# Kernel tuning notes

Measured on AMD Instinct MI355X. Metric: run time of the kernel, lower is better.

The kernel has to match this reference:

```python
import jax, jax.numpy as jnp
import numpy as np

DIM = 256
HEADS = 8
H = 32
W = 32
N = H * W  # must equal 4*DIM for the BatchNorm1d(dim*4) over the token dim to be valid
TAU = 2.0
V_TH = 1.0


def _rope_rotations():
    # RoPE buffer: shape (H, W, DIM//2) angles; k_max = DIM // (2*2)
    k_max = DIM // 4
    theta = 1.0 / (10000.0 ** (jnp.arange(k_max, dtype=jnp.float32) / k_max))
    hg, wg = jnp.meshgrid(jnp.arange(H, dtype=jnp.float32), jnp.arange(W, dtype=jnp.float32), indexing='ij')
    angles = jnp.concatenate([hg[..., None] * theta, wg[..., None] * theta], axis=-1)  # (H,W,DIM//2)
    return jnp.cos(angles), jnp.sin(angles)


def _apply_rope(x, cos, sin):
    # x: (b,H,W,DIM); complex rotation on consecutive (re,im) pairs
    x2 = x.reshape(*x.shape[:-1], -1, 2)
    re, im = x2[..., 0], x2[..., 1]
    out = jnp.stack([cos * re - sin * im, sin * re + cos * im], axis=-1)
    return out.reshape(x.shape)


def _lif(x):
    # MultiStepLIFNode(tau=2.0, detach_reset=True): time axis = axis 0 (here batch, as in source),
    # decay_input=True, v_reset=0 (hard reset), heaviside fwd + sigmoid(alpha=4) surrogate bwd.
    def step(v, xt):
        v = v + (xt - v) / TAU
        sg = jax.nn.sigmoid(4.0 * (v - V_TH))
        spike = jax.lax.stop_gradient((v >= V_TH).astype(x.dtype) - sg) + sg
        v = v * (1.0 - jax.lax.stop_gradient(spike))  # detach_reset hard reset to 0
        return v, spike
    _, s = jax.lax.scan(step, jnp.zeros_like(x[0]), x)
    return s


def setup_inputs() -> dict:
    key = jax.random.key(0)
    ks = jax.random.split(key, 4)
    x = jax.random.normal(ks[0], (8, N, DIM), dtype=jnp.float32)
    Wqk = jax.random.normal(ks[1], (DIM, 2 * DIM), dtype=jnp.float32) * 0.02
    bqk = jnp.zeros((2 * DIM,), dtype=jnp.float32)
    bn_gamma = jnp.ones((N,), dtype=jnp.float32)
    bn_beta = jnp.zeros((N,), dtype=jnp.float32)
    lepe_w = jax.random.normal(ks[2], (DIM, 1, 3, 3), dtype=jnp.float32) * 0.1
    lepe_b = jnp.zeros((DIM,), dtype=jnp.float32)
    return {"x": x, "Wqk": Wqk, "bqk": bqk, "bn_gamma": bn_gamma, "bn_beta": bn_beta,
            "lepe_w": lepe_w, "lepe_b": lepe_b}


def reference(x, Wqk, bqk, bn_gamma, bn_beta, lepe_w, lepe_b):
    b, n, c = x.shape
    hd = c // HEADS
    cos, sin = _rope_rotations()

    qk = x @ Wqk + bqk  # (b,n,2c)
    # Dropout is identity in eval. BatchNorm1d(4*dim) in eval mode: channels = token dim (n == 4*dim),
    # running_mean=0, running_var=1 -> pure affine per token index.
    qk = qk * bn_gamma[None, :, None] + bn_beta[None, :, None]
    qk = _lif(qk)
    q, k = qk[..., :c], qk[..., c:]  # reshape(b,n,2,c) split
    v = x
    q = jax.nn.elu(q) + 1.0
    k = jax.nn.elu(k) + 1.0

    q_rope = _apply_rope(q.reshape(b, H, W, c), cos, sin).reshape(b, n, HEADS, hd).transpose(0, 2, 1, 3)
    k_rope = _apply_rope(k.reshape(b, H, W, c), cos, sin).reshape(b, n, HEADS, hd).transpose(0, 2, 1, 3)
    qh = q.reshape(b, n, HEADS, hd).transpose(0, 2, 1, 3)  # (b,h,n,d)
    kh = k.reshape(b, n, HEADS, hd).transpose(0, 2, 1, 3)
    vh = v.reshape(b, n, HEADS, hd).transpose(0, 2, 1, 3)

    atten = jnp.einsum('bhnd,bhmd->bhnm', qh, kh)  # returned, not used for output
    kmean = kh.mean(axis=2, keepdims=True)  # (b,h,1,d)
    z = 1.0 / (jnp.einsum('bhnd,bhed->bhne', qh, kmean) + 1e-6)  # (b,h,n,1)
    kv = jnp.einsum('bhnd,bhne->bhde', k_rope, vh) / n  # (k^T n^-0.5) @ (v n^-0.5)
    out = jnp.einsum('bhnd,bhde->bhne', q_rope, kv) * z  # (b,h,n,d)
    out = out.transpose(0, 2, 1, 3).reshape(b, n, c)

    v_img = vh.transpose(0, 2, 1, 3).reshape(b, H, W, c).transpose(0, 3, 1, 2)  # (b,c,H,W)
    lepe = jax.lax.conv_general_dilated(v_img, lepe_w, (1, 1), 'SAME',
                                        feature_group_count=c,
                                        dimension_numbers=('NCHW', 'OIHW', 'NCHW'))
    lepe = lepe + lepe_b[None, :, None, None]
    out = out + lepe.transpose(0, 2, 3, 1).reshape(b, n, c)
    return (out, qh, kh, v_img, atten)
```

## Files before the change

kernel.cpp:

```cpp
#include <hip/hip_runtime.h>
#include <cstdint>
#include <cstddef>

#define OFF_OUT   0
#define OFF_QH    2097152
#define OFF_KH    4194304
#define OFF_VIMG  6291456
#define OFF_ATT   8388608

#define WS_MQ   0
#define WS_MK   65536
#define WS_TBL  131072
#define WS_KVP  393216
#define WS_KMP  655360

typedef float f32x4 __attribute__((ext_vector_type(4)));

__device__ __forceinline__ int wcol(int g) { return g * 8 + 4 * (g >> 2); }

__device__ __forceinline__ void gemm_lif_256(
    const float* __restrict__ x, const float* __restrict__ Wqk,
    const float* __restrict__ bqk, const float* __restrict__ gamma,
    const float* __restrict__ beta, unsigned* __restrict__ mq,
    unsigned* __restrict__ mk, float* pool,
    int blk_n, int blk_c, int t)
{
    const int ks = t >> 7, tl = t & 127;
    const int c_t = tl & 15, n_l = tl >> 4;
    const int n0 = blk_n * 8, c0 = blk_c * 128;
    float* wpool = pool + ks * 4480;
    float* xpool = pool + 8960 + ks * 2176;

    float acc[8][8];
    #pragma unroll
    for (int b = 0; b < 8; ++b)
        #pragma unroll
        for (int j = 0; j < 8; ++j) acc[b][j] = 0.f;

    const int um = tl >> 3, ukq = tl & 7;
    const float* gx0 = x + ((size_t)(um & 7) * 1024 + n0 + (um >> 3)) * 256
                         + ks * 128 + ukq * 4;
    const float* gw0 = Wqk + (size_t)(ks * 128 + (tl >> 5)) * 512 + c0 + (tl & 31) * 4;
    const int wg = (tl & 31) >> 1;
    float* lw_ = wpool + (tl >> 5) * 140 + wcol(wg) + (tl & 1) * 4;
    float* lx_ = xpool + (ukq * 4) * 68 + um;

    f32x4 px[4], pw[8];
    #pragma unroll
    for (int i = 0; i < 4; ++i) px[i] = *(const f32x4*)(gx0 + (size_t)(i * 2) * 256);
    #pragma unroll
    for (int i = 0; i < 8; ++i) pw[i] = *(const f32x4*)(gw0 + (size_t)(i * 4) * 512);

    for (int p = 0; p < 4; ++p) {
        #pragma unroll
        for (int i = 0; i < 4; ++i)
            #pragma unroll
            for (int j = 0; j < 4; ++j)
                lx_[j * 68 + i * 16] = px[i][j];
        #pragma unroll
        for (int i = 0; i < 8; ++i)
            *(f32x4*)(lw_ + i * 4 * 140) = pw[i];
        __syncthreads();
        if (p < 3) {
            int ko = (p + 1) * 32;
            #pragma unroll
            for (int i = 0; i < 4; ++i)
                px[i] = *(const f32x4*)(gx0 + (size_t)(i * 2) * 256 + ko);
            #pragma unroll
            for (int i = 0; i < 8; ++i)
                pw[i] = *(const f32x4*)(gw0 + (size_t)(ko + i * 4) * 512);
        }
        const int xc = n_l * 8;
        const int wc = wcol(c_t);
        #pragma unroll 8
        for (int kk = 0; kk < 32; ++kk) {
            f32x4 xa = *(const f32x4*)(xpool + kk * 68 + xc);
            f32x4 xb = *(const f32x4*)(xpool + kk * 68 + xc + 4);
            f32x4 wa = *(const f32x4*)(wpool + kk * 140 + wc);
            f32x4 wb = *(const f32x4*)(wpool + kk * 140 + wc + 4);
            #pragma unroll
            for (int b = 0; b < 4; ++b) {
                #pragma unroll
                for (int j = 0; j < 4; ++j) {
                    acc[b][j]         = fmaf(xa[b], wa[j], acc[b][j]);
                    acc[b][j + 4]     = fmaf(xa[b], wb[j], acc[b][j + 4]);
                    acc[b + 4][j]     = fmaf(xb[b], wa[j], acc[b + 4][j]);
                    acc[b + 4][j + 4] = fmaf(xb[b], wb[j], acc[b + 4][j + 4]);
                }
            }
        }
        __syncthreads();
    }

    float* comb = pool;
    if (ks == 1) {
        #pragma unroll
        for (int b = 0; b < 8; ++b)
            #pragma unroll
            for (int j = 0; j < 8; ++j)
                comb[(b * 8 + j) * 129 + tl] = acc[b][j];
    }
    __syncthreads();
    unsigned char* nib = (unsigned char*)(pool + 8960);
    if (ks == 0) {
        #pragma unroll
        for (int b = 0; b < 8; ++b)
            #pragma unroll
            for (int j = 0; j < 8; ++j)
                acc[b][j] += comb[(b * 8 + j) * 129 + tl];
        float g = gamma[n0 + n_l], be = beta[n0 + n_l];
        f32x4 bqa = *(const f32x4*)(bqk + c0 + c_t * 8);
        f32x4 bqb = *(const f32x4*)(bqk + c0 + c_t * 8 + 4);
        float v[8];
        #pragma unroll
        for (int j = 0; j < 8; ++j) v[j] = 0.f;
        #pragma unroll
        for (int b = 0; b < 8; ++b) {
            unsigned byte = 0;
            #pragma unroll
            for (int j = 0; j < 8; ++j) {
                float bqv = (j < 4) ? bqa[j] : bqb[j - 4];
                float a = (acc[b][j] + bqv) * g + be;
                v[j] = v[j] + (a - v[j]) * 0.5f;
                bool sp = (v[j] >= 1.f);
                v[j] = sp ? 0.f : v[j];
                byte |= (sp ? 1u : 0u) << j;
            }
            nib[n_l * 128 + c_t * 8 + b] = (unsigned char)byte;
        }
    }
    __syncthreads();
    {
        int b = t & 7, w = (t >> 3) & 3, nl = t >> 5;
        unsigned wd = 0;
        #pragma unroll
        for (int j = 0; j < 4; ++j)
            wd |= (unsigned)nib[nl * 128 + (w * 4 + j) * 8 + b] << (8 * j);
        unsigned h = (unsigned)((blk_c & 1) * 4 + w);
        unsigned* dst = (blk_c < 2) ? mq : mk;
        dst[b * 8192 + h * 1024 + n0 + nl] = wd;
    }
}

__global__ __launch_bounds__(256) void phaseA_kernel(
    const float* __restrict__ x, const float* __restrict__ Wqk,
    const float* __restrict__ bqk, const float* __restrict__ gamma,
    const float* __restrict__ beta, unsigned* __restrict__ mq,
    unsigned* __restrict__ mk, float* __restrict__ vimg,
    float* __restrict__ tbl)
{
    __shared__ float smem[13312];
    int t = threadIdx.x;
    int blk = blockIdx.x;
    if (blk < 256) {
        gemm_lif_256(x, Wqk, bqk, gamma, beta, mq, mk, smem,
                     blk >> 1, 2 + (blk & 1), t);
        return;
    }
    if (blk >= 2304) {
        int id = (blk - 2304) * 256 + t;
        int j = id & 127, n = id >> 7;
        int i = (j < 64) ? j : j - 64;
        float th = powf(10000.0f, -(float)i * (1.0f / 64.0f));
        float pos = (float)((j < 64) ? (n >> 5) : (n & 31));
        float ang = pos * th;
        tbl[n * 256 + j * 2]     = cosf(ang);
        tbl[n * 256 + j * 2 + 1] = sinf(ang);
        return;
    }
    float* s = smem;
    int tile = blk - 256;
    int b = tile >> 8, ti = tile & 255;
    int p0 = (ti >> 3) * 32, c0 = (ti & 7) * 32;
    int row = t >> 3, c4 = (t & 7) * 4;
    const float4 vl = *(const float4*)&x[(b * 1024 + p0 + row) * 256 + c0 + c4];
    s[row * 33 + c4 + 0] = vl.x; s[row * 33 + c4 + 1] = vl.y;
    s[row * 33 + c4 + 2] = vl.z; s[row * 33 + c4 + 3] = vl.w;
    __syncthreads();
    int cc = t >> 3, p4 = (t & 7) * 4;
    f32x4 o;
    o.x = s[(p4 + 0) * 33 + cc]; o.y = s[(p4 + 1) * 33 + cc];
    o.z = s[(p4 + 2) * 33 + cc]; o.w = s[(p4 + 3) * 33 + cc];
    *(f32x4*)&vimg[(b * 256 + c0 + cc) * 1024 + p0 + p4] = o;
}

__global__ __launch_bounds__(256) void phaseB_kernel(
    const float* __restrict__ x, const float* __restrict__ Wqk,
    const float* __restrict__ bqk, const float* __restrict__ gamma,
    const float* __restrict__ beta, unsigned* __restrict__ mq,
    unsigned* __restrict__ mk, const float* __restrict__ tbl,
    float* __restrict__ kvp, float* __restrict__ kmp)
{
    __shared__ float smem[13312];
    int t = threadIdx.x;
    int blk = blockIdx.x;
    if (blk < 256) {
        gemm_lif_256(x, Wqk, bqk, gamma, beta, mq, mk, smem,
                     blk >> 1, blk & 1, t);
        return;
    }
    int unit = blk - 256;
    int bh = unit >> 2, seg = unit & 3;
    int b = bh >> 3, h = bh & 7;
    int n0 = seg * 256;
    float* kr   = smem;
    float* vhs  = smem + 2304;
    float* part = smem + 4416;
    int d = t & 31, ch = t >> 5;
    int sc = 0;
    for (int i = 0; i < 32; ++i)
        sc += (mk[bh * 1024 + n0 + ch * 32 + i] >> d) & 1u;
    part[ch * 32 + d] = (float)sc;
    __syncthreads();
    if (t < 32) {
        float cs = 0.f;
        #pragma unroll
        for (int j = 0; j < 8; ++j) cs += part[j * 32 + t];
        kmp[bh * 128 + seg * 32 + t] = cs;
    }
    float a0 = 0, a1 = 0, a2 = 0, a3 = 0;
    int e = t & 31, db = (t >> 5) * 4;
    for (int c0 = n0; c0 < n0 + 256; c0 += 64) {
        __syncthreads();
        #pragma unroll
        for (int i = 0; i < 8; ++i) {
            int f = t + i * 256;
            int nn = f >> 5, dd = f & 31;
            int n = c0 + nn;
            unsigned w = mk[bh * 1024 + n];
            float kd = 1.0f + (float)((w >> dd) & 1u);
            float ko = 1.0f + (float)((w >> (dd ^ 1)) & 1u);
            const float* cp = tbl + n * 256 + h * 32 + (dd & ~1);
            float cc2 = cp[0], ss2 = cp[1];
            kr[nn * 36 + dd] = (dd & 1) ? (ss2 * ko + cc2 * kd) : (cc2 * kd - ss2 * ko);
            vhs[nn * 33 + dd] = x[(b * 1024 + n) * 256 + h * 32 + dd];
        }
        __syncthreads();
        #pragma unroll 8
        for (int nn = 0; nn < 64; ++nn) {
            float ve = vhs[nn * 33 + e];
            float4 kk = *(const float4*)&kr[nn * 36 + db];
            a0 = fmaf(kk.x, ve, a0); a1 = fmaf(kk.y, ve, a1);
            a2 = fmaf(kk.z, ve, a2); a3 = fmaf(kk.w, ve, a3);
        }
    }
    float* dst = kvp + bh * 4096 + seg * 1024;
    dst[(db + 0) * 32 + e] = a0;
    dst[(db + 1) * 32 + e] = a1;
    dst[(db + 2) * 32 + e] = a2;
    dst[(db + 3) * 32 + e] = a3;
}

__global__ __launch_bounds__(256) void phaseC_kernel(
    const unsigned* __restrict__ mq, const unsigned* __restrict__ mk,
    const float* __restrict__ x, const float* __restrict__ tbl,
    const float* __restrict__ kvp, const float* __restrict__ kmp,
    const float* __restrict__ lw, const float* __restrict__ lb,
    float* __restrict__ outbase)
{
    int t = threadIdx.x;
    if (blockIdx.x >= 512) {
        int blk = blockIdx.x - 512;
        int bh = blk >> 5;
        int tile = blk & 31;
        float* qh = outbase + OFF_QH;
        float* kh = outbase + OFF_KH;
        float* att = outbase + OFF_ATT;
        {
            int row = tile * 32 + (t >> 3);
            int d0 = (t & 7) * 4;
            unsigned wq = mq[bh * 1024 + row], wk = mk[bh * 1024 + row];
            f32x4 a, bb;
            a.x = 1.f + (float)((wq >> (d0 + 0)) & 1u);
            a.y = 1.f + (float)((wq >> (d0 + 1)) & 1u);
            a.z = 1.f + (float)((wq >> (d0 + 2)) & 1u);
            a.w = 1.f + (float)((wq >> (d0 + 3)) & 1u);
            bb.x = 1.f + (float)((wk >> (d0 + 0)) & 1u);
            bb.y = 1.f + (float)((wk >> (d0 + 1)) & 1u);
            bb.z = 1.f + (float)((wk >> (d0 + 2)) & 1u);
            bb.w = 1.f + (float)((wk >> (d0 + 3)) & 1u);
            *(f32x4*)&qh[((bh * 1024 + row) << 5) + d0] = a;
            *(f32x4*)&kh[((bh * 1024 + row) << 5) + d0] = bb;
        }
        uint4 mm = ((const uint4*)(mk + bh * 1024))[t];
        float4 rr;
        rr.x = (float)__popc(mm.x); rr.y = (float)__popc(mm.y);
        rr.z = (float)__popc(mm.z); rr.w = (float)__popc(mm.w);
        float* base = att + ((size_t)bh * 1024 + (size_t)tile * 32) * 1024;
        const unsigned* mqrow = mq + bh * 1024 + tile * 32;
        for (int row = 0; row < 32; ++row) {
            unsigned mqw = mqrow[row];
            float rq = 32.0f + (float)__popc(mqw);
            f32x4 o;
            o.x = rq + rr.x + (float)__popc(mqw & mm.x);
            o.y = rq + rr.y + (float)__popc(mqw & mm.y);
            o.z = rq + rr.z + (float)__popc(mqw & mm.z);
            o.w = rq + rr.w + (float)__popc(mqw & mm.w);
            ((f32x4*)(base + (size_t)row * 1024))[t] = o;
        }
        return;
    }
    int bi = blockIdx.x;
    int bh = bi >> 3, sub = bi & 7;
    int pseg = sub >> 1, half = sub & 1;
    int b = bh >> 3, h = bh & 7;
    bool hy = (h < 4);
    int e = t & 31, p_l = t >> 5;
    int p = pseg * 8 + p_l;
    int q0 = half * 16;
    float* out = outbase + OFF_OUT;

    __shared__ float kvs[32][32];
    __shared__ float kmf[32];
    __shared__ float zs[128];
    const float inv = 1.0f / 1024.0f;
    #pragma unroll
    for (int i = 0; i < 4; ++i) {
        int f = t + i * 256;
        const float* kp = kvp + bh * 4096 + f;
        kvs[f >> 5][f & 31] = (kp[0] + kp[1024] + kp[2048] + kp[3072]) * inv;
    }
    if (t < 32) {
        const float* mp = kmp + bh * 128 + t;
        kmf[t] = 1.0f + (mp[0] + mp[32] + mp[64] + mp[96]) * inv;
    }
    __syncthreads();
    float S = 0.f;
    #pragma unroll
    for (int dd = 0; dd < 32; ++dd) S += kmf[dd];
    if (t < 128) {
        int pl2 = t >> 4, iq = t & 15;
        int pp = pseg * 8 + pl2, qq = q0 + iq;
        int n = hy ? (pp * 32 + qq) : (qq * 32 + pp);
        unsigned w = mq[bh * 1024 + n];
        float acc = S;
        #pragma unroll
        for (int dd = 0; dd < 32; ++dd)
            acc += (float)((w >> dd) & 1u) * kmf[dd];
        zs[t] = 1.0f / (acc + 1e-6f);
    }
    int n_ref = hy ? (p * 32) : p;
    const float* cp = tbl + n_ref * 256 + h * 32;
    float E[16], O[16], B = 0.f;
    #pragma unroll
    for (int j = 0; j < 16; ++j) {
        float c2 = cp[2 * j], s2 = cp[2 * j + 1];
        float K0 = kvs[2 * j][e], K1 = kvs[2 * j + 1][e];
        E[j] = c2 * K0 + s2 * K1;
        O[j] = c2 * K1 - s2 * K0;
        B += E[j] + O[j];
    }
    __syncthreads();
    int c = h * 32 + e;
    float w9[9];
    #pragma unroll
    for (int j = 0; j < 9; ++j) w9[j] = lw[c * 9 + j];
    float lbv = lb[c];
    const float* xb = x + (size_t)b * 262144 + c;
    auto ld = [&](int yy, int xx) -> float {
        if ((unsigned)yy > 31u || (unsigned)xx > 31u) return 0.f;
        return xb[(yy * 32 + xx) * 256];
    };
    if (hy) {
        int y = p;
        float Wm0 = ld(y - 1, q0 - 1), Wm1 = ld(y, q0 - 1), Wm2 = ld(y + 1, q0 - 1);
        float Wc0 = ld(y - 1, q0),     Wc1 = ld(y, q0),     Wc2 = ld(y + 1, q0);
        #pragma unroll 4
        for (int i = 0; i < 16; ++i) {
            int m = q0 + i;
            float Wp0 = ld(y - 1, m + 1), Wp1 = ld(y, m + 1), Wp2 = ld(y + 1, m + 1);
            int n = y * 32 + m;
            unsigned w = mq[bh * 1024 + n];
            float o = B;
            #pragma unroll
            for (int j = 0; j < 16; ++j) {
                o += (float)((w >> (2 * j)) & 1u) * E[j];
                o += (float)((w >> (2 * j + 1)) & 1u) * O[j];
            }
            o *= zs[p_l * 16 + i];
            float l = lbv;
            l = fmaf(w9[0], Wm0, l); l = fmaf(w9[1], Wc0, l); l = fmaf(w9[2], Wp0, l);
            l = fmaf(w9[3], Wm1, l); l = fmaf(w9[4], Wc1, l); l = fmaf(w9[5], Wp1, l);
            l = fmaf(w9[6], Wm2, l); l = fmaf(w9[7], Wc2, l); l = fmaf(w9[8], Wp2, l);
            out[((b * 1024 + n) << 8) + c] = o + l;
            Wm0 = Wc0; Wm1 = Wc1; Wm2 = Wc2;
            Wc0 = Wp0; Wc1 = Wp1; Wc2 = Wp2;
        }
    } else {
        int xx0 = p;
        float Wm0 = ld(q0 - 1, xx0 - 1), Wm1 = ld(q0 - 1, xx0), Wm2 = ld(q0 - 1, xx0 + 1);
        float Wc0 = ld(q0, xx0 - 1),     Wc1 = ld(q0, xx0),     Wc2 = ld(q0, xx0 + 1);
        #pragma unroll 4
        for (int i = 0; i < 16; ++i) {
            int m = q0 + i;
            float Wp0 = ld(m + 1, xx0 - 1), Wp1 = ld(m + 1, xx0), Wp2 = ld(m + 1, xx0 + 1);
            int n = m * 32 + xx0;
            unsigned w = mq[bh * 1024 + n];
            float o = B;
            #pragma unroll
            for (int j = 0; j < 16; ++j) {
                o += (float)((w >> (2 * j)) & 1u) * E[j];
                o += (float)((w >> (2 * j + 1)) & 1u) * O[j];
            }
            o *= zs[p_l * 16 + i];
            float l = lbv;
            l = fmaf(w9[0], Wm0, l); l = fmaf(w9[1], Wm1, l); l = fmaf(w9[2], Wm2, l);
            l = fmaf(w9[3], Wc0, l); l = fmaf(w9[4], Wc1, l); l = fmaf(w9[5], Wc2, l);
            l = fmaf(w9[6], Wp0, l); l = fmaf(w9[7], Wp1, l); l = fmaf(w9[8], Wp2, l);
            out[((b * 1024 + n) << 8) + c] = o + l;
            Wm0 = Wc0; Wm1 = Wc1; Wm2 = Wc2;
            Wc0 = Wp0; Wc1 = Wp1; Wc2 = Wp2;
        }
    }
}

extern "C" void kernel_launch(void* const* d_in, const int* in_sizes, int n_in,
                              void* d_out, int out_size, void* d_ws, size_t ws_size,
                              hipStream_t stream)
{
    const float* x     = (const float*)d_in[0];
    const float* Wqk   = (const float*)d_in[1];
    const float* bqk   = (const float*)d_in[2];
    const float* gamma = (const float*)d_in[3];
    const float* beta  = (const float*)d_in[4];
    const float* lw    = (const float*)d_in[5];
    const float* lb    = (const float*)d_in[6];
    float* out = (float*)d_out;
    unsigned* ws = (unsigned*)d_ws;
    unsigned* mq = ws + WS_MQ;
    unsigned* mk = ws + WS_MK;
    float* tbl  = (float*)(ws + WS_TBL);
    float* kvp  = (float*)(ws + WS_KVP);
    float* kmp  = (float*)(ws + WS_KMP);

    hipLaunchKernelGGL(phaseA_kernel, dim3(2816), dim3(256), 0, stream,
                       x, Wqk, bqk, gamma, beta, mq, mk, out + OFF_VIMG, tbl);
    hipLaunchKernelGGL(phaseB_kernel, dim3(512), dim3(256), 0, stream,
                       x, Wqk, bqk, gamma, beta, mq, mk, tbl, kvp, kmp);
    hipLaunchKernelGGL(phaseC_kernel, dim3(2560), dim3(256), 0, stream,
                       mq, mk, x, tbl, kvp, kmp, lw, lb, out);
}
```

Measured before the change: 95.30 us.

## Reschedule phases: all GEMM+LIF first, then attention-map with kv partials, then output

All four GEMM+LIF column groups now run in the first kernel alongside the v_img transpose and RoPE table. The second kernel overlaps the large attention-map/qh/kh writes with the kv-partial and key-mean reduction. The final kernel computes only the output. This rebalances work across launches so the memory-bound attention store hides the kv compute, and the attention loop now preloads the 32 q mask words into registers. The first launch grows heavier, and the register array may raise register pressure.

Result: slower. 103.5 us (+8.6%).

```diff
diff --git a/kernel.cpp b/kernel.cpp
--- a/kernel.cpp
+++ b/kernel.cpp
@@ -142,7 +142,7 @@
     }
 }
 
-__global__ __launch_bounds__(256) void phaseA_kernel(
+__global__ __launch_bounds__(256) void l1_kernel(
     const float* __restrict__ x, const float* __restrict__ Wqk,
     const float* __restrict__ bqk, const float* __restrict__ gamma,
     const float* __restrict__ beta, unsigned* __restrict__ mq,
@@ -152,13 +152,13 @@
     __shared__ float smem[13312];
     int t = threadIdx.x;
     int blk = blockIdx.x;
-    if (blk < 256) {
+    if (blk < 512) {
         gemm_lif_256(x, Wqk, bqk, gamma, beta, mq, mk, smem,
-                     blk >> 1, 2 + (blk & 1), t);
+                     blk >> 2, blk & 3, t);
         return;
     }
-    if (blk >= 2304) {
-        int id = (blk - 2304) * 256 + t;
+    if (blk >= 2560) {
+        int id = (blk - 2560) * 256 + t;
         int j = id & 127, n = id >> 7;
         int i = (j < 64) ? j : j - 64;
         float th = powf(10000.0f, -(float)i * (1.0f / 64.0f));
@@ -169,7 +169,7 @@
         return;
     }
     float* s = smem;
-    int tile = blk - 256;
+    int tile = blk - 512;
     int b = tile >> 8, ti = tile & 255;
     int p0 = (ti >> 3) * 32, c0 = (ti & 7) * 32;
     int row = t >> 3, c4 = (t & 7) * 4;
@@ -184,83 +184,15 @@
     *(f32x4*)&vimg[(b * 256 + c0 + cc) * 1024 + p0 + p4] = o;
 }
 
-__global__ __launch_bounds__(256) void phaseB_kernel(
-    const float* __restrict__ x, const float* __restrict__ Wqk,
-    const float* __restrict__ bqk, const float* __restrict__ gamma,
-    const float* __restrict__ beta, unsigned* __restrict__ mq,
-    unsigned* __restrict__ mk, const float* __restrict__ tbl,
-    float* __restrict__ kvp, float* __restrict__ kmp)
-{
-    __shared__ float smem[13312];
-    int t = threadIdx.x;
-    int blk = blockIdx.x;
-    if (blk < 256) {
-        gemm_lif_256(x, Wqk, bqk, gamma, beta, mq, mk, smem,
-                     blk >> 1, blk & 1, t);
-        return;
-    }
-    int unit = blk - 256;
-    int bh = unit >> 2, seg = unit & 3;
-    int b = bh >> 3, h = bh & 7;
-    int n0 = seg * 256;
-    float* kr   = smem;
-    float* vhs  = smem + 2304;
-    float* part = smem + 4416;
-    int d = t & 31, ch = t >> 5;
-    int sc = 0;
-    for (int i = 0; i < 32; ++i)
-        sc += (mk[bh * 1024 + n0 + ch * 32 + i] >> d) & 1u;
-    part[ch * 32 + d] = (float)sc;
-    __syncthreads();
-    if (t < 32) {
-        float cs = 0.f;
-        #pragma unroll
-        for (int j = 0; j < 8; ++j) cs += part[j * 32 + t];
-        kmp[bh * 128 + seg * 32 + t] = cs;
-    }
-    float a0 = 0, a1 = 0, a2 = 0, a3 = 0;
-    int e = t & 31, db = (t >> 5) * 4;
-    for (int c0 = n0; c0 < n0 + 256; c0 += 64) {
-        __syncthreads();
-        #pragma unroll
-        for (int i = 0; i < 8; ++i) {
-            int f = t + i * 256;
-            int nn = f >> 5, dd = f & 31;
-            int n = c0 + nn;
-            unsigned w = mk[bh * 1024 + n];
-            float kd = 1.0f + (float)((w >> dd) & 1u);
-            float ko = 1.0f + (float)((w >> (dd ^ 1)) & 1u);
-            const float* cp = tbl + n * 256 + h * 32 + (dd & ~1);
-            float cc2 = cp[0], ss2 = cp[1];
-            kr[nn * 36 + dd] = (dd & 1) ? (ss2 * ko + cc2 * kd) : (cc2 * kd - ss2 * ko);
-            vhs[nn * 33 + dd] = x[(b * 1024 + n) * 256 + h * 32 + dd];
-        }
-        __syncthreads();
-        #pragma unroll 8
-        for (int nn = 0; nn < 64; ++nn) {
-            float ve = vhs[nn * 33 + e];
-            float4 kk = *(const float4*)&kr[nn * 36 + db];
-            a0 = fmaf(kk.x, ve, a0); a1 = fmaf(kk.y, ve, a1);
-            a2 = fmaf(kk.z, ve, a2); a3 = fmaf(kk.w, ve, a3);
-        }
-    }
-    float* dst = kvp + bh * 4096 + seg * 1024;
-    dst[(db + 0) * 32 + e] = a0;
-    dst[(db + 1) * 32 + e] = a1;
-    dst[(db + 2) * 32 + e] = a2;
-    dst[(db + 3) * 32 + e] = a3;
-}
-
-__global__ __launch_bounds__(256) void phaseC_kernel(
+__global__ __launch_bounds__(256) void l2_kernel(
     const unsigned* __restrict__ mq, const unsigned* __restrict__ mk,
     const float* __restrict__ x, const float* __restrict__ tbl,
-    const float* __restrict__ kvp, const float* __restrict__ kmp,
-    const float* __restrict__ lw, const float* __restrict__ lb,
+    float* __restrict__ kvp, float* __restrict__ kmp,
     float* __restrict__ outbase)
 {
     int t = threadIdx.x;
-    if (blockIdx.x >= 512) {
-        int blk = blockIdx.x - 512;
+    if (blockIdx.x < 2048) {
+        int blk = blockIdx.x;
         int bh = blk >> 5;
         int tile = blk & 31;
         float* qh = outbase + OFF_QH;
@@ -286,20 +218,84 @@
         float4 rr;
         rr.x = (float)__popc(mm.x); rr.y = (float)__popc(mm.y);
         rr.z = (float)__popc(mm.z); rr.w = (float)__popc(mm.w);
+        const unsigned* mqrow = mq + bh * 1024 + tile * 32;
+        unsigned mqw[32];
+        #pragma unroll
+        for (int r = 0; r < 32; ++r) mqw[r] = mqrow[r];
         float* base = att + ((size_t)bh * 1024 + (size_t)tile * 32) * 1024;
-        const unsigned* mqrow = mq + bh * 1024 + tile * 32;
+        #pragma unroll 4
         for (int row = 0; row < 32; ++row) {
-            unsigned mqw = mqrow[row];
-            float rq = 32.0f + (float)__popc(mqw);
+            unsigned w = mqw[row];
+            float rq = 32.0f + (float)__popc(w);
             f32x4 o;
-            o.x = rq + rr.x + (float)__popc(mqw & mm.x);
-            o.y = rq + rr.y + (float)__popc(mqw & mm.y);
-            o.z = rq + rr.z + (float)__popc(mqw & mm.z);
-            o.w = rq + rr.w + (float)__popc(mqw & mm.w);
+            o.x = rq + rr.x + (float)__popc(w & mm.x);
+            o.y = rq + rr.y + (float)__popc(w & mm.y);
+            o.z = rq + rr.z + (float)__popc(w & mm.z);
+            o.w = rq + rr.w + (float)__popc(w & mm.w);
             ((f32x4*)(base + (size_t)row * 1024))[t] = o;
         }
         return;
     }
+    __shared__ float smem[4800];
+    int unit = blockIdx.x - 2048;
+    int bh = unit >> 2, seg = unit & 3;
+    int b = bh >> 3, h = bh & 7;
+    int n0 = seg * 256;
+    float* kr   = smem;
+    float* vhs  = smem + 2304;
+    float* part = smem + 4416;
+    int d = t & 31, ch = t >> 5;
+    int sc = 0;
+    for (int i = 0; i < 32; ++i)
+        sc += (mk[bh * 1024 + n0 + ch * 32 + i] >> d) & 1u;
+    part[ch * 32 + d] = (float)sc;
+    __syncthreads();
+    if (t < 32) {
+        float cs = 0.f;
+        #pragma unroll
+        for (int j = 0; j < 8; ++j) cs += part[j * 32 + t];
+        kmp[bh * 128 + seg * 32 + t] = cs;
+    }
+    float a0 = 0, a1 = 0, a2 = 0, a3 = 0;
+    int e = t & 31, db = (t >> 5) * 4;
+    for (int c0 = n0; c0 < n0 + 256; c0 += 64) {
+        __syncthreads();
+        #pragma unroll
+        for (int i = 0; i < 8; ++i) {
+            int f = t + i * 256;
+            int nn = f >> 5, dd = f & 31;
+            int n = c0 + nn;
+            unsigned w = mk[bh * 1024 + n];
+            float kd = 1.0f + (float)((w >> dd) & 1u);
+            float ko = 1.0f + (float)((w >> (dd ^ 1)) & 1u);
+            const float* cp = tbl + n * 256 + h * 32 + (dd & ~1);
+            float cc2 = cp[0], ss2 = cp[1];
+            kr[nn * 36 + dd] = (dd & 1) ? (ss2 * ko + cc2 * kd) : (cc2 * kd - ss2 * ko);
+            vhs[nn * 33 + dd] = x[(b * 1024 + n) * 256 + h * 32 + dd];
+        }
+        __syncthreads();
+        #pragma unroll 8
+        for (int nn = 0; nn < 64; ++nn) {
+            float ve = vhs[nn * 33 + e];
+            float4 kk = *(const float4*)&kr[nn * 36 + db];
+            a0 = fmaf(kk.x, ve, a0); a1 = fmaf(kk.y, ve, a1);
+            a2 = fmaf(kk.z, ve, a2); a3 = fmaf(kk.w, ve, a3);
+        }
+    }
+    float* dst = kvp + bh * 4096 + seg * 1024;
+    dst[(db + 0) * 32 + e] = a0;
+    dst[(db + 1) * 32 + e] = a1;
+    dst[(db + 2) * 32 + e] = a2;
+    dst[(db + 3) * 32 + e] = a3;
+}
+
+__global__ __launch_bounds__(256) void l3_kernel(
+    const unsigned* __restrict__ mq, const float* __restrict__ x,
+    const float* __restrict__ tbl, const float* __restrict__ kvp,
+    const float* __restrict__ kmp, const float* __restrict__ lw,
+    const float* __restrict__ lb, float* __restrict__ out)
+{
+    int t = threadIdx.x;
     int bi = blockIdx.x;
     int bh = bi >> 3, sub = bi & 7;
     int pseg = sub >> 1, half = sub & 1;
@@ -308,7 +304,6 @@
     int e = t & 31, p_l = t >> 5;
     int p = pseg * 8 + p_l;
     int q0 = half * 16;
-    float* out = outbase + OFF_OUT;
 
     __shared__ float kvs[32][32];
     __shared__ float kmf[32];
@@ -433,10 +428,10 @@
     float* kvp  = (float*)(ws + WS_KVP);
     float* kmp  = (float*)(ws + WS_KMP);
 
-    hipLaunchKernelGGL(phaseA_kernel, dim3(2816), dim3(256), 0, stream,
+    hipLaunchKernelGGL(l1_kernel, dim3(3072), dim3(256), 0, stream,
                        x, Wqk, bqk, gamma, beta, mq, mk, out + OFF_VIMG, tbl);
-    hipLaunchKernelGGL(phaseB_kernel, dim3(512), dim3(256), 0, stream,
-                       x, Wqk, bqk, gamma, beta, mq, mk, tbl, kvp, kmp);
-    hipLaunchKernelGGL(phaseC_kernel, dim3(2560), dim3(256), 0, stream,
-                       mq, mk, x, tbl, kvp, kmp, lw, lb, out);
+    hipLaunchKernelGGL(l2_kernel, dim3(2304), dim3(256), 0, stream,
+                       mq, mk, x, tbl, kvp, kmp, out);
+    hipLaunchKernelGGL(l3_kernel, dim3(512), dim3(256), 0, stream,
+                       mq, x, tbl, kvp, kmp, lw, lb, out + OFF_OUT);
 }
```

## Move attention-matrix writes into phase B GEMM blocks, shrink phase C grid

Applied to the files above, without the earlier changes.

The phase B blocks that compute the Q spike masks now keep their packed mask words in shared memory and write the corresponding atten rows directly, reading the K masks that phase A already produced. Phase C no longer writes atten. Its extra blocks now only expand the qh/kh masks to floats using a flat, coalesced indexing, so its grid drops from 2560 to 1024 blocks. The goal is to overlap the large atten store with the phase B attention-stat blocks and cut phase C's tail, at the cost of heavier, possibly unbalanced GEMM blocks in phase B.

New measurement: 106.2 us. +11.4%, slower.

```diff
diff --git a/kernel.cpp b/kernel.cpp
--- a/kernel.cpp
+++ b/kernel.cpp
@@ -22,7 +22,7 @@
     const float* __restrict__ x, const float* __restrict__ Wqk,
     const float* __restrict__ bqk, const float* __restrict__ gamma,
     const float* __restrict__ beta, unsigned* __restrict__ mq,
-    unsigned* __restrict__ mk, float* pool,
+    unsigned* __restrict__ mk, float* pool, unsigned* wlds,
     int blk_n, int blk_c, int t)
 {
     const int ks = t >> 7, tl = t & 127;
@@ -139,6 +139,7 @@
         unsigned h = (unsigned)((blk_c & 1) * 4 + w);
         unsigned* dst = (blk_c < 2) ? mq : mk;
         dst[b * 8192 + h * 1024 + n0 + nl] = wd;
+        if (wlds) wlds[nl * 32 + w * 8 + b] = wd;
     }
 }
 
@@ -153,7 +154,7 @@
     int t = threadIdx.x;
     int blk = blockIdx.x;
     if (blk < 256) {
-        gemm_lif_256(x, Wqk, bqk, gamma, beta, mq, mk, smem,
+        gemm_lif_256(x, Wqk, bqk, gamma, beta, mq, mk, smem, nullptr,
                      blk >> 1, 2 + (blk & 1), t);
         return;
     }
@@ -189,14 +190,43 @@
     const float* __restrict__ bqk, const float* __restrict__ gamma,
     const float* __restrict__ beta, unsigned* __restrict__ mq,
     unsigned* __restrict__ mk, const float* __restrict__ tbl,
-    float* __restrict__ kvp, float* __restrict__ kmp)
+    float* __restrict__ kvp, float* __restrict__ kmp,
+    float* __restrict__ att)
 {
     __shared__ float smem[13312];
     int t = threadIdx.x;
     int blk = blockIdx.x;
     if (blk < 256) {
-        gemm_lif_256(x, Wqk, bqk, gamma, beta, mq, mk, smem,
-                     blk >> 1, blk & 1, t);
+        int blk_n = blk >> 1, blk_c = blk & 1;
+        unsigned* wlds = (unsigned*)smem;
+        gemm_lif_256(x, Wqk, bqk, gamma, beta, mq, mk, smem, wlds,
+                     blk_n, blk_c, t);
+        __syncthreads();
+        int n0 = blk_n * 8;
+        int hbase = blk_c * 4;
+        #pragma unroll
+        for (int hp = 0; hp < 4; ++hp) {
+            int h = hbase + hp;
+            #pragma unroll
+            for (int b = 0; b < 8; ++b) {
+                int bh = b * 8 + h;
+                uint4 mm = ((const uint4*)(mk + bh * 1024))[t];
+                float r0 = (float)__popc(mm.x), r1 = (float)__popc(mm.y);
+                float r2 = (float)__popc(mm.z), r3 = (float)__popc(mm.w);
+                float* base = att + ((size_t)bh * 1024 + n0) * 1024;
+                #pragma unroll
+                for (int nl = 0; nl < 8; ++nl) {
+                    unsigned w = wlds[nl * 32 + hp * 8 + b];
+                    float rq = 32.0f + (float)__popc(w);
+                    f32x4 o;
+                    o.x = rq + r0 + (float)__popc(w & mm.x);
+                    o.y = rq + r1 + (float)__popc(w & mm.y);
+                    o.z = rq + r2 + (float)__popc(w & mm.z);
+                    o.w = rq + r3 + (float)__popc(w & mm.w);
+                    ((f32x4*)(base + (size_t)nl * 1024))[t] = o;
+                }
+            }
+        }
         return;
     }
     int unit = blk - 256;
@@ -260,43 +290,21 @@
 {
     int t = threadIdx.x;
     if (blockIdx.x >= 512) {
-        int blk = blockIdx.x - 512;
-        int bh = blk >> 5;
-        int tile = blk & 31;
-        float* qh = outbase + OFF_QH;
-        float* kh = outbase + OFF_KH;
-        float* att = outbase + OFF_ATT;
-        {
-            int row = tile * 32 + (t >> 3);
-            int d0 = (t & 7) * 4;
-            unsigned wq = mq[bh * 1024 + row], wk = mk[bh * 1024 + row];
-            f32x4 a, bb;
-            a.x = 1.f + (float)((wq >> (d0 + 0)) & 1u);
-            a.y = 1.f + (float)((wq >> (d0 + 1)) & 1u);
-            a.z = 1.f + (float)((wq >> (d0 + 2)) & 1u);
-            a.w = 1.f + (float)((wq >> (d0 + 3)) & 1u);
-            bb.x = 1.f + (float)((wk >> (d0 + 0)) & 1u);
-            bb.y = 1.f + (float)((wk >> (d0 + 1)) & 1u);
-            bb.z = 1.f + (float)((wk >> (d0 + 2)) & 1u);
-            bb.w = 1.f + (float)((wk >> (d0 + 3)) & 1u);
-            *(f32x4*)&qh[((bh * 1024 + row) << 5) + d0] = a;
-            *(f32x4*)&kh[((bh * 1024 + row) << 5) + d0] = bb;
-        }
-        uint4 mm = ((const uint4*)(mk + bh * 1024))[t];
-        float4 rr;
-        rr.x = (float)__popc(mm.x); rr.y = (float)__popc(mm.y);
-        rr.z = (float)__popc(mm.z); rr.w = (float)__popc(mm.w);
-        float* base = att + ((size_t)bh * 1024 + (size_t)tile * 32) * 1024;
-        const unsigned* mqrow = mq + bh * 1024 + tile * 32;
-        for (int row = 0; row < 32; ++row) {
-            unsigned mqw = mqrow[row];
-            float rq = 32.0f + (float)__popc(mqw);
+        int blk2 = blockIdx.x - 512;
+        #pragma unroll
+        for (int j = 0; j < 8; ++j) {
+            int qi = blk2 * 2048 + j * 256 + t;
+            int tensor = qi >> 19;
+            int rr = qi & 524287;
+            const unsigned* m = tensor ? mk : mq;
+            unsigned w = m[rr >> 3];
+            int d0 = (rr & 7) * 4;
             f32x4 o;
-            o.x = rq + rr.x + (float)__popc(mqw & mm.x);
-            o.y = rq + rr.y + (float)__popc(mqw & mm.y);
-            o.z = rq + rr.z + (float)__popc(mqw & mm.z);
-            o.w = rq + rr.w + (float)__popc(mqw & mm.w);
-            ((f32x4*)(base + (size_t)row * 1024))[t] = o;
+            o.x = 1.0f + (float)((w >> (d0 + 0)) & 1u);
+            o.y = 1.0f + (float)((w >> (d0 + 1)) & 1u);
+            o.z = 1.0f + (float)((w >> (d0 + 2)) & 1u);
+            o.w = 1.0f + (float)((w >> (d0 + 3)) & 1u);
+            ((f32x4*)(outbase + (tensor ? OFF_KH : OFF_QH)))[rr] = o;
         }
         return;
     }
@@ -436,7 +444,8 @@
     hipLaunchKernelGGL(phaseA_kernel, dim3(2816), dim3(256), 0, stream,
                        x, Wqk, bqk, gamma, beta, mq, mk, out + OFF_VIMG, tbl);
     hipLaunchKernelGGL(phaseB_kernel, dim3(512), dim3(256), 0, stream,
-                       x, Wqk, bqk, gamma, beta, mq, mk, tbl, kvp, kmp);
-    hipLaunchKernelGGL(phaseC_kernel, dim3(2560), dim3(256), 0, stream,
+                       x, Wqk, bqk, gamma, beta, mq, mk, tbl, kvp, kmp,
+                       out + OFF_ATT);
+    hipLaunchKernelGGL(phaseC_kernel, dim3(1024), dim3(256), 0, stream,
                        mq, mk, x, tbl, kvp, kmp, lw, lb, out);
 }
```
